# Kernel tuning notes

Hardware: AMD Instinct MI355X
Metric: run time of the kernel (lower is better)

## Reference

```python
import jax, jax.numpy as jnp
import numpy as np


def _pairwise_sqdist(x, y):
    # x: [B, N, D], y: [B, M, D] -> P: [B, N, M] squared euclidean distances
    xx = jnp.sum(x * x, axis=-1)              # [B, N]
    yy = jnp.sum(y * y, axis=-1)              # [B, M]
    zz = jnp.einsum('bnd,bmd->bnm', x, y)     # [B, N, M]
    return xx[:, :, None] + yy[:, None, :] - 2.0 * zz


def setup_inputs() -> dict:
    key = jax.random.key(0)
    k1, k2 = jax.random.split(key)
    B, N, D = 8, 8192, 3
    preds = jax.random.normal(k1, (B, N, D), dtype=jnp.float32)
    gts = jax.random.normal(k2, (B, N, D), dtype=jnp.float32)
    return {"preds": preds, "gts": gts}


def reference(preds, gts):
    # P = batch_pairwise_dist(gts, preds): P[b, i, j] = ||gts[b,i] - preds[b,j]||^2
    P = _pairwise_sqdist(gts, preds)          # [B, N_gts, N_preds]
    loss_1 = jnp.sum(jnp.min(P, axis=1))      # min over gts points
    loss_2 = jnp.sum(jnp.min(P, axis=2))      # min over pred points
    return loss_1 + loss_2
```

## Files before the change

### kernel.cpp

```cpp
#include <hip/hip_runtime.h>

typedef _Float16 f16;
typedef f16 half8 __attribute__((ext_vector_type(8)));
typedef float f32x16 __attribute__((ext_vector_type(16)));

#define BB 8
#define NN 8192
#define SETPTS (BB * NN)
#define NPTS (2 * SETPTS)
#define TQ NPTS

__device__ __forceinline__ void gload_lds16(const void* g, void* l) {
  __builtin_amdgcn_global_load_lds(
      (const __attribute__((address_space(1))) void*)g,
      (__attribute__((address_space(3))) void*)l, 16, 0, 0);
}

__global__ __launch_bounds__(256) void chamfer_prep(
    const float* __restrict__ preds, const float* __restrict__ gts,
    float* __restrict__ yy, half8* __restrict__ Aq, half8* __restrict__ Bq) {
  int idx = blockIdx.x * 256 + threadIdx.x;
  int s = idx >> 16;
  int off = idx & (SETPTS - 1);
  const float* src = s ? gts : preds;
  float x0 = src[off * 3 + 0], x1 = src[off * 3 + 1], x2 = src[off * 3 + 2];

  f16 h0 = (f16)x0; f16 l0 = (f16)(x0 - (float)h0);
  f16 h1 = (f16)x1; f16 l1 = (f16)(x1 - (float)h1);
  f16 h2 = (f16)x2; f16 l2 = (f16)(x2 - (float)h2);

  float Y0 = -2.f * x0, Y1 = -2.f * x1, Y2 = -2.f * x2;
  f16 H0 = (f16)Y0; f16 L0 = (f16)(Y0 - (float)H0);
  f16 H1 = (f16)Y1; f16 L1 = (f16)(Y1 - (float)H1);
  f16 H2 = (f16)Y2; f16 L2 = (f16)(Y2 - (float)H2);

  float yv = x0 * x0 + x1 * x1 + x2 * x2;
  f16 yh = (f16)yv; f16 yl = (f16)(yv - (float)yh);

  f16 one = (f16)1.f, zz = (f16)0.f;
  half8 A0 = {h0, l0, h0, l0, h1, l1, h1, l1};
  half8 A1 = {h2, l2, h2, l2, one, one, zz, zz};
  half8 B0 = {H0, H0, L0, L0, H1, H1, L1, L1};
  half8 B1 = {H2, H2, L2, L2, yh, yl, zz, zz};

  Aq[idx * 2 + 0] = A0; Aq[idx * 2 + 1] = A1;
  Bq[idx * 2 + 0] = B0; Bq[idx * 2 + 1] = B1;
  yy[idx] = yv;
}

template <int R>
__global__ __launch_bounds__(256, 4) void chamfer_mfma(
    const half8* __restrict__ Aq, const half8* __restrict__ Bq,
    float* __restrict__ partial) {
  constexpr int NSTEP = NN / R / 32;
  constexpr int CH = 16;
  constexpr int NCH = NSTEP / CH;
  __shared__ __align__(16) char lds[2][CH * 1024];

  int bi = blockIdx.x;
  int xcd = bi & 7;
  int idx = bi >> 3;
  int panel = xcd * 2 + (idx & 1);
  int dir = panel >> 3;
  int b = panel & 7;
  int sub = idx >> 1;
  int qb = sub & 31;
  int r = sub >> 5;

  int tid = threadIdx.x;
  int w = tid >> 6;
  int l = tid & 63;
  int l31 = l & 31;
  int lh = l >> 5;

  const half8* Ap =
      Aq + ((size_t)(dir * BB + b) * NN + qb * 256 + w * 64) * 2;
  half8 a0 = Ap[l31 * 2 + lh];
  half8 a1 = Ap[(32 + l31) * 2 + lh];

  const char* gpanel = (const char*)(Bq + ((size_t)((1 - dir) * BB + b) * NN +
                                           r * (NN / R)) * 2);
  int perm = ((l & 31) * 2 + (l >> 5)) * 16;

  auto stage = [&](int buf, int c) {
    const char* csrc = gpanel + (size_t)(c * CH + w * 4) * 1024 + perm;
    char* cdst = &lds[buf][w * 4 * 1024];
#pragma unroll
    for (int i = 0; i < 4; ++i)
      gload_lds16(csrc + i * 1024, cdst + i * 1024);
  };

  f32x16 zero;
#pragma unroll
  for (int i = 0; i < 16; ++i) zero[i] = 0.f;
  f32x16 run0, run1;
#pragma unroll
  for (int i = 0; i < 16; ++i) { run0[i] = 3.4e38f; run1[i] = 3.4e38f; }

  stage(0, 0);
  __syncthreads();

#pragma unroll 1
  for (int ch = 0; ch < NCH; ++ch) {
    int par = ch & 1;
    if (ch + 1 < NCH) stage(par ^ 1, ch + 1);
    const half8* lb = (const half8*)&lds[par][0];
#pragma unroll 4
    for (int st = 0; st < CH; ++st) {
      half8 bt = lb[st * 64 + l];
      f32x16 o0 = __builtin_amdgcn_mfma_f32_32x32x16_f16(a0, bt, zero, 0, 0, 0);
      f32x16 o1 = __builtin_amdgcn_mfma_f32_32x32x16_f16(a1, bt, zero, 0, 0, 0);
#pragma unroll
      for (int i = 0; i < 16; ++i) {
        run0[i] = fminf(run0[i], o0[i]);
        run1[i] = fminf(run1[i], o1[i]);
      }
    }
    __syncthreads();
  }

  size_t qflat = (size_t)(dir * BB + b) * NN + qb * 256 + w * 64;
  float* pr = partial + (size_t)r * TQ + qflat;
#pragma unroll
  for (int i = 0; i < 16; ++i) {
    float v0 = run0[i], v1 = run1[i];
    v0 = fminf(v0, __shfl_xor(v0, 1));  v1 = fminf(v1, __shfl_xor(v1, 1));
    v0 = fminf(v0, __shfl_xor(v0, 2));  v1 = fminf(v1, __shfl_xor(v1, 2));
    v0 = fminf(v0, __shfl_xor(v0, 4));  v1 = fminf(v1, __shfl_xor(v1, 4));
    v0 = fminf(v0, __shfl_xor(v0, 8));  v1 = fminf(v1, __shfl_xor(v1, 8));
    v0 = fminf(v0, __shfl_xor(v0, 16)); v1 = fminf(v1, __shfl_xor(v1, 16));
    int row = (i & 3) + 8 * (i >> 2) + 4 * lh;
    if (l31 == i) {
      pr[row] = v0;
      pr[32 + row] = v1;
    }
  }
}

template <int R>
__global__ __launch_bounds__(256) void chamfer_combine(
    const float* __restrict__ partial, const float* __restrict__ yy,
    float* __restrict__ bsums) {
  int q = blockIdx.x * 256 + threadIdx.x;
  float m = partial[q];
#pragma unroll
  for (int rr = 1; rr < R; ++rr) m = fminf(m, partial[(size_t)rr * TQ + q]);
  m += yy[q];
  __shared__ float s[256];
  s[threadIdx.x] = m;
  __syncthreads();
  for (int o = 128; o > 0; o >>= 1) {
    if (threadIdx.x < o) s[threadIdx.x] += s[threadIdx.x + o];
    __syncthreads();
  }
  if (threadIdx.x == 0) bsums[blockIdx.x] = s[0];
}

__global__ __launch_bounds__(256) void chamfer_final(
    const float* __restrict__ bsums, float* __restrict__ out, int n) {
  float v = 0.f;
  for (int i = threadIdx.x; i < n; i += 256) v += bsums[i];
  __shared__ float s[256];
  s[threadIdx.x] = v;
  __syncthreads();
  for (int o = 128; o > 0; o >>= 1) {
    if (threadIdx.x < o) s[threadIdx.x] += s[threadIdx.x + o];
    __syncthreads();
  }
  if (threadIdx.x == 0) out[0] = s[0];
}

extern "C" void kernel_launch(void* const* d_in, const int* in_sizes, int n_in,
                              void* d_out, int out_size, void* d_ws,
                              size_t ws_size, hipStream_t stream) {
  const float* preds = (const float*)d_in[0];
  const float* gts = (const float*)d_in[1];
  float* out = (float*)d_out;

  float* partial = (float*)d_ws;
  float* bsums = partial + (size_t)2 * TQ;
  float* yy = bsums + 1024;
  half8* Aq = (half8*)(yy + NPTS);
  half8* Bq = Aq + (size_t)NPTS * 2;

  chamfer_prep<<<NPTS / 256, 256, 0, stream>>>(preds, gts, yy, Aq, Bq);
  chamfer_mfma<2><<<2 * BB * 32 * 2, 256, 0, stream>>>(Aq, Bq, partial);
  chamfer_combine<2><<<TQ / 256, 256, 0, stream>>>(partial, yy, bsums);
  chamfer_final<<<1, 256, 0, stream>>>(bsums, out, TQ / 256);
}
```

Baseline: 52.82 us.

## Swap MFMA operands so min reduction runs within-lane over accumulator registers

Swaps the A and B operands of the 32x32 MFMA so query points land on output columns and reference points on rows. Each lane can then min-reduce its 16 accumulator values with a tree of fminf into one scalar running minimum, replacing two 16-wide running-min vectors. This frees many VGPRs and shortens the epilogue to a single cross-half shuffle. The inner-loop fminf count stays roughly the same, but register pressure and the final reduction shrink.

```diff
diff --git a/kernel.cpp b/kernel.cpp
--- a/kernel.cpp
+++ b/kernel.cpp
@@ -73,10 +73,10 @@
   int l31 = l & 31;
   int lh = l >> 5;
 
-  const half8* Ap =
+  const half8* Qp =
       Aq + ((size_t)(dir * BB + b) * NN + qb * 256 + w * 64) * 2;
-  half8 a0 = Ap[l31 * 2 + lh];
-  half8 a1 = Ap[(32 + l31) * 2 + lh];
+  half8 q0 = Qp[l31 * 2 + lh];
+  half8 q1 = Qp[(32 + l31) * 2 + lh];
 
   const char* gpanel = (const char*)(Bq + ((size_t)((1 - dir) * BB + b) * NN +
                                            r * (NN / R)) * 2);
@@ -93,9 +93,7 @@
   f32x16 zero;
 #pragma unroll
   for (int i = 0; i < 16; ++i) zero[i] = 0.f;
-  f32x16 run0, run1;
-#pragma unroll
-  for (int i = 0; i < 16; ++i) { run0[i] = 3.4e38f; run1[i] = 3.4e38f; }
+  float run0 = 3.4e38f, run1 = 3.4e38f;
 
   stage(0, 0);
   __syncthreads();
@@ -108,32 +106,40 @@
 #pragma unroll 4
     for (int st = 0; st < CH; ++st) {
       half8 bt = lb[st * 64 + l];
-      f32x16 o0 = __builtin_amdgcn_mfma_f32_32x32x16_f16(a0, bt, zero, 0, 0, 0);
-      f32x16 o1 = __builtin_amdgcn_mfma_f32_32x32x16_f16(a1, bt, zero, 0, 0, 0);
-#pragma unroll
-      for (int i = 0; i < 16; ++i) {
-        run0[i] = fminf(run0[i], o0[i]);
-        run1[i] = fminf(run1[i], o1[i]);
+      f32x16 oa = __builtin_amdgcn_mfma_f32_32x32x16_f16(bt, q0, zero, 0, 0, 0);
+      f32x16 ob = __builtin_amdgcn_mfma_f32_32x32x16_f16(bt, q1, zero, 0, 0, 0);
+      {
+        float t0 = fminf(fminf(oa[0], oa[1]), oa[2]);
+        float t1 = fminf(fminf(oa[3], oa[4]), oa[5]);
+        float t2 = fminf(fminf(oa[6], oa[7]), oa[8]);
+        float t3 = fminf(fminf(oa[9], oa[10]), oa[11]);
+        float t4 = fminf(fminf(oa[12], oa[13]), oa[14]);
+        float u0 = fminf(fminf(t0, t1), t2);
+        float u1 = fminf(fminf(t3, t4), oa[15]);
+        run0 = fminf(fminf(run0, u0), u1);
+      }
+      {
+        float t0 = fminf(fminf(ob[0], ob[1]), ob[2]);
+        float t1 = fminf(fminf(ob[3], ob[4]), ob[5]);
+        float t2 = fminf(fminf(ob[6], ob[7]), ob[8]);
+        float t3 = fminf(fminf(ob[9], ob[10]), ob[11]);
+        float t4 = fminf(fminf(ob[12], ob[13]), ob[14]);
+        float u0 = fminf(fminf(t0, t1), t2);
+        float u1 = fminf(fminf(t3, t4), ob[15]);
+        run1 = fminf(fminf(run1, u0), u1);
       }
     }
     __syncthreads();
   }
 
+  float v0 = fminf(run0, __shfl_xor(run0, 32));
+  float v1 = fminf(run1, __shfl_xor(run1, 32));
+
   size_t qflat = (size_t)(dir * BB + b) * NN + qb * 256 + w * 64;
   float* pr = partial + (size_t)r * TQ + qflat;
-#pragma unroll
-  for (int i = 0; i < 16; ++i) {
-    float v0 = run0[i], v1 = run1[i];
-    v0 = fminf(v0, __shfl_xor(v0, 1));  v1 = fminf(v1, __shfl_xor(v1, 1));
-    v0 = fminf(v0, __shfl_xor(v0, 2));  v1 = fminf(v1, __shfl_xor(v1, 2));
-    v0 = fminf(v0, __shfl_xor(v0, 4));  v1 = fminf(v1, __shfl_xor(v1, 4));
-    v0 = fminf(v0, __shfl_xor(v0, 8));  v1 = fminf(v1, __shfl_xor(v1, 8));
-    v0 = fminf(v0, __shfl_xor(v0, 16)); v1 = fminf(v1, __shfl_xor(v1, 16));
-    int row = (i & 3) + 8 * (i >> 2) + 4 * lh;
-    if (l31 == i) {
-      pr[row] = v0;
-      pr[32 + row] = v1;
-    }
+  if (lh == 0) {
+    pr[l31] = v0;
+    pr[32 + l31] = v1;
   }
 }
 
```

Result: faster. 46.23 us (-12.5%).
